# Kernel optimization log

Hardware: AMD Instinct MI355X
Metric: run time of the kernel (lower is better)

## Reference

```python
import math
import jax, jax.numpy as jnp
import numpy as np

B, NPC, K, D, T, L = 512, 32, 12, 64, 64, 4  # crystals, atoms/crystal, knn, node_dim, time_dim, layers
N = B * NPC
E_IN = 2 * D + 1 + T   # 193
N_IN = 2 * D + T       # 192


def setup_inputs() -> dict:
    key = jax.random.key(0)
    ks = jax.random.split(key, 32)
    rn = lambda k, shp, s=0.05: jax.random.normal(k, shp, jnp.float32) * s
    inp = {}
    inp["z_nodes"] = jax.random.normal(ks[0], (N, 128), jnp.float32)
    inp["t"] = jax.random.uniform(ks[1], (B,), jnp.float32) * 1000.0
    inp["frac_coords"] = jax.random.uniform(ks[2], (N, 3), jnp.float32)
    inp["lattice"] = jnp.eye(3, dtype=jnp.float32) * 5.0 + rn(ks[3], (B, 3, 3), 0.3)
    inp["batch_indices"] = jnp.repeat(jnp.arange(B, dtype=jnp.int32), NPC)
    inp["num_atoms"] = NPC
    # time_mlp: Linear(T, 2T) -> SiLU -> Linear(2T, T)
    inp["time_w1"] = rn(ks[4], (T, 2 * T)); inp["time_b1"] = rn(ks[5], (2 * T,))
    inp["time_w2"] = rn(ks[6], (2 * T, T)); inp["time_b2"] = rn(ks[7], (T,))
    # node_embedding: Linear(128, D)
    inp["emb_w"] = rn(ks[8], (128, D)); inp["emb_b"] = rn(ks[9], (D,))
    # per-layer EGNN params stacked on leading L axis
    inp["edge_w1"] = rn(ks[10], (L, E_IN, D)); inp["edge_b1"] = rn(ks[11], (L, D))
    inp["edge_w2"] = rn(ks[12], (L, D, D));    inp["edge_b2"] = rn(ks[13], (L, D))
    inp["coord_w1"] = rn(ks[14], (L, D, D));   inp["coord_b1"] = rn(ks[15], (L, D))
    inp["coord_w2"] = rn(ks[16], (L, D, 1))
    inp["node_w1"] = rn(ks[17], (L, N_IN, D)); inp["node_b1"] = rn(ks[18], (L, D))
    inp["node_w2"] = rn(ks[19], (L, D, D));    inp["node_b2"] = rn(ks[20], (L, D))
    return inp


def _forward(z_nodes, t, frac_coords, lattice, batch_indices, num_atoms,
             time_w1, time_b1, time_w2, time_b2, emb_w, emb_b,
             edge_w1, edge_b1, edge_w2, edge_b2, coord_w1, coord_b1, coord_w2,
             node_w1, node_b1, node_w2, node_b2):
    silu = jax.nn.silu
    n = num_atoms
    b = lattice.shape[0]
    n_nodes = z_nodes.shape[0]

    # ---- time embedding ----
    half = T // 2
    freqs = jnp.exp(jnp.arange(half, dtype=jnp.float32) * (-math.log(10000.0) / (half - 1)))
    ang = t[:, None] * freqs[None, :]
    sinu = jnp.concatenate([jnp.sin(ang), jnp.cos(ang)], axis=-1)  # [B, T]
    t_feat = silu(sinu @ time_w1 + time_b1) @ time_w2 + time_b2     # [B, T]
    t_nodes = t_feat[batch_indices]                                  # [N, T]

    h = z_nodes @ emb_w + emb_b                                      # [N, D]

    # ---- vectorized PBC KNN graph (all crystals have n atoms) ----
    f = frac_coords.reshape(b, n, 3)
    diff_f = f[:, :, None, :] - f[:, None, :, :]
    diff_f = diff_f - jnp.round(diff_f)
    diff_c = jnp.einsum('bijk,bkl->bijl', diff_f, lattice)           # [b,n,n,3]
    dist_sq = jnp.sum(diff_c * diff_c, axis=-1)                      # [b,n,n]
    dist_sq = jnp.where(jnp.eye(n, dtype=bool)[None], jnp.inf, dist_sq)
    k = min(K, n - 1)
    _, idx = jax.lax.top_k(-dist_sq, k)                              # [b,n,k] neighbor indices
    offs = (jnp.arange(b, dtype=jnp.int32) * n)[:, None, None]
    edge_src = (idx + offs).reshape(-1)                              # neighbors j
    edge_dst = (jnp.broadcast_to(jnp.arange(n, dtype=jnp.int32)[None, :, None], (b, n, k)) + offs).reshape(-1)
    diff_cart = jnp.take_along_axis(diff_c, jnp.broadcast_to(idx[..., None], (b, n, k, 3)), axis=2).reshape(-1, 3)
    dist_sq_e = jnp.take_along_axis(dist_sq, idx, axis=2).reshape(-1, 1)

    t_edges = t_nodes[edge_src]                                      # [E, T]

    total_shift = jnp.zeros((n_nodes, 3), dtype=h.dtype)
    for l in range(L):
        edge_in = jnp.concatenate([h[edge_src], h[edge_dst], dist_sq_e, t_edges], axis=-1)
        m = silu(edge_in @ edge_w1[l] + edge_b1[l])
        m = silu(m @ edge_w2[l] + edge_b2[l])                        # [E, D]
        cw = silu(m @ coord_w1[l] + coord_b1[l]) @ coord_w2[l]       # [E, 1]
        coord_update = jax.ops.segment_sum(diff_cart * cw, edge_src, num_segments=n_nodes)
        m_i = jax.ops.segment_sum(m, edge_dst, num_segments=n_nodes)
        node_in = jnp.concatenate([h, m_i, t_nodes], axis=-1)
        h = h + (silu(node_in @ node_w1[l] + node_b1[l]) @ node_w2[l] + node_b2[l])
        total_shift = total_shift + coord_update

    inv_lat = jnp.linalg.inv(lattice)[batch_indices]                 # [N,3,3]
    shift_frac = jnp.einsum('ni,nij->nj', total_shift, inv_lat)
    return shift_frac, h


def reference(z_nodes, t, frac_coords, lattice, batch_indices, num_atoms,
              time_w1, time_b1, time_w2, time_b2, emb_w, emb_b,
              edge_w1, edge_b1, edge_w2, edge_b2, coord_w1, coord_b1, coord_w2,
              node_w1, node_b1, node_w2, node_b2):
    return _forward(z_nodes, t, frac_coords, lattice, batch_indices, num_atoms,
                    time_w1, time_b1, time_w2, time_b2, emb_w, emb_b,
                    edge_w1, edge_b1, edge_w2, edge_b2, coord_w1, coord_b1, coord_w2,
                    node_w1, node_b1, node_w2, node_b2)
```

## Files before the change

### kernel.cpp

```cpp
#include <hip/hip_runtime.h>
#include <hip/hip_bf16.h>
#include <math.h>

#define NB 512
#define NPC 32
#define KNN 12
#define NL 4
#define NN (NB*NPC)
#define WPL 28672

typedef float v4f __attribute__((ext_vector_type(4)));
typedef short s8v __attribute__((ext_vector_type(8)));

__device__ __forceinline__ float silu_f(float x) {
    return x * __builtin_amdgcn_rcpf(1.0f + __builtin_amdgcn_exp2f(x * -1.44269504088896341f));
}

__device__ __forceinline__ unsigned short f2bf(float x) {
    unsigned u = __float_as_uint(x);
    u += 0x7fffu + ((u >> 16) & 1u);
    return (unsigned short)(u >> 16);
}

__device__ __forceinline__ unsigned pk2bf(float a, float b) {
    __hip_bfloat162 t = __float22bfloat162_rn(make_float2(a, b));
    union { __hip_bfloat162 h; unsigned u; } c; c.h = t;
    return c.u;
}

__device__ __forceinline__ int div12(int e) { return (e * 1366) >> 14; }

template<int R>
__device__ __forceinline__ void gemm_acc(const float* A, int astride,
                                         const float* __restrict__ Wg,
                                         int K, int lane, float* acc) {
#pragma unroll 2
    for (int kq = 0; kq < (K >> 2); ++kq) {
        float w0 = Wg[(4*kq+0)*64 + lane];
        float w1 = Wg[(4*kq+1)*64 + lane];
        float w2 = Wg[(4*kq+2)*64 + lane];
        float w3 = Wg[(4*kq+3)*64 + lane];
#pragma unroll
        for (int r = 0; r < R; ++r) {
            float4 a = *(const float4*)(A + r*astride + 4*kq);
            acc[r] = fmaf(a.x, w0, acc[r]);
            acc[r] = fmaf(a.y, w1, acc[r]);
            acc[r] = fmaf(a.z, w2, acc[r]);
            acc[r] = fmaf(a.w, w3, acc[r]);
        }
    }
}

extern "C" __global__ void prepack_w(const float* __restrict__ edge_w1, const float* __restrict__ edge_w2,
                                     const float* __restrict__ coord_w1, const float* __restrict__ node_w1,
                                     const float* __restrict__ node_w2, unsigned short* __restrict__ wout) {
    int g = blockIdx.x * 256 + threadIdx.x;
    if (g >= 4 * WPL / 8) return;
    int l = (g * 8) / WPL;
    int r = (g * 8) % WPL;
    int base, nKt, mat;
    if      (r < 8192)  { base = 0;     nKt = 2; mat = 0; }
    else if (r < 12288) { base = 8192;  nKt = 2; mat = 1; }
    else if (r < 16384) { base = 12288; nKt = 2; mat = 2; }
    else if (r < 24576) { base = 16384; nKt = 4; mat = 3; }
    else                { base = 24576; nKt = 2; mat = 4; }
    int idx = r - base;
    int lane = (idx >> 3) & 63, t = idx >> 9;
    int kt = t % nKt, nt = t / nKt;
    int k0 = kt*32 + ((lane >> 4) & 3)*8;
    int n  = nt*16 + (lane & 15);
    unsigned short o[8];
#pragma unroll
    for (int j = 0; j < 8; ++j) {
        int k = k0 + j;
        float v;
        if      (mat == 0) v = (n < 64) ? edge_w1[l*193*64 + k*64 + n] : edge_w1[l*193*64 + (64+k)*64 + (n-64)];
        else if (mat == 1) v = edge_w2 [l*4096 + k*64 + n];
        else if (mat == 2) v = coord_w1[l*4096 + k*64 + n];
        else if (mat == 3) v = node_w1 [l*192*64 + k*64 + n];
        else               v = node_w2 [l*4096 + k*64 + n];
        o[j] = f2bf(v);
    }
    *(s8v*)(wout + g*8) = *(s8v*)o;
}

extern "C" __global__ __launch_bounds__(512, 2)
void crystal_fused(const float* __restrict__ z_nodes, const float* __restrict__ t_in,
                   const float* __restrict__ frac,    const float* __restrict__ lattice,
                   const float* __restrict__ time_w1, const float* __restrict__ time_b1,
                   const float* __restrict__ time_w2, const float* __restrict__ time_b2,
                   const float* __restrict__ emb_w,   const float* __restrict__ emb_b,
                   const float* __restrict__ edge_w1, const float* __restrict__ edge_b1,
                   const float* __restrict__ edge_b2, const float* __restrict__ coord_b1,
                   const float* __restrict__ coord_w2,
                   const float* __restrict__ node_w1, const float* __restrict__ node_b1,
                   const float* __restrict__ node_b2,
                   const unsigned short* __restrict__ wbf,
                   float* __restrict__ out)
{
    __shared__ __align__(16) float s_h[32*65];
    __shared__ __align__(16) unsigned short s_habf[32*136];
    __shared__ __align__(16) unsigned short s_n1bf[32*72];
    __shared__ __align__(16) float s_hs[32*68];
    __shared__ __align__(16) float s_hd[32*68];
    __shared__ __align__(16) unsigned short s_tiles16[8*1152];
    __shared__ float s_dsq[32][33];
    __shared__ float2 s_emeta[384];
    __shared__ float s_endc[384*3];
    __shared__ float s_frac[32][3];
    __shared__ float s_lat[9], s_inv[9];
    __shared__ float s_sinu[64], s_t1[128], s_tf[64];
    __shared__ float s_tb4[NL*64], s_nb4[NL*64];
    __shared__ float s_shift[32*3];

    const int tid  = threadIdx.x;
    const int c    = blockIdx.x;
    const int lane = tid & 63;
    const int wave = tid >> 6;
    const int q4   = lane >> 4;
    const int c16  = lane & 15;
    const int base = c * NPC;

    if (tid < 96) {
        ((float*)s_frac)[tid] = frac[base*3 + tid];
    } else if (tid < 105) {
        s_lat[tid-96] = lattice[c*9 + (tid-96)];
    } else if (tid >= 128 && tid < 160) {
        int i = tid - 128;
        float freq = expf((float)i * (-9.210340371976184f / 31.0f));
        float ang  = t_in[c] * freq;
        s_sinu[i]    = sinf(ang);
        s_sinu[i+32] = cosf(ang);
    }
    __syncthreads();

    float* dcf = (float*)s_tiles16;
    {
        float l00=s_lat[0],l01=s_lat[1],l02=s_lat[2];
        float l10=s_lat[3],l11=s_lat[4],l12=s_lat[5];
        float l20=s_lat[6],l21=s_lat[7],l22=s_lat[8];
        for (int p = tid; p < 1024; p += 512) {
            int i = p >> 5, j = p & 31;
            float dx = s_frac[i][0]-s_frac[j][0];
            float dy = s_frac[i][1]-s_frac[j][1];
            float dz = s_frac[i][2]-s_frac[j][2];
            dx -= rintf(dx); dy -= rintf(dy); dz -= rintf(dz);
            float cx = dx*l00 + dy*l10 + dz*l20;
            float cy = dx*l01 + dy*l11 + dz*l21;
            float cz = dx*l02 + dy*l12 + dz*l22;
            float dd = cx*cx + cy*cy + cz*cz;
            s_dsq[i][j] = (i==j) ? 3.0e38f : dd;
            dcf[p*3+0]=cx; dcf[p*3+1]=cy; dcf[p*3+2]=cz;
        }
    }
    __syncthreads();

    if (tid < 32) {
        int i = tid;
        for (int k = 0; k < KNN; ++k) {
            float best = 3.9e38f; int bj = 0;
            for (int j = 0; j < 32; ++j) {
                float v = s_dsq[i][j];
                if (v < best) { best = v; bj = j; }
            }
            s_dsq[i][bj] = 3.9e38f;
            int e = i*KNN + k;
            s_emeta[e] = make_float2(best, __int_as_float(bj));
            int p = (i<<5) + bj;
            s_endc[e*3+0] = dcf[p*3+0];
            s_endc[e*3+1] = dcf[p*3+1];
            s_endc[e*3+2] = dcf[p*3+2];
        }
    } else if (tid >= 128 && tid < 256) {
        int jj = tid - 128;
        float p0 = time_b1[jj], p1=0.f, p2=0.f, p3=0.f;
        for (int k = 0; k < 64; k += 4) {
            p0 = fmaf(s_sinu[k+0], time_w1[(k+0)*128+jj], p0);
            p1 = fmaf(s_sinu[k+1], time_w1[(k+1)*128+jj], p1);
            p2 = fmaf(s_sinu[k+2], time_w1[(k+2)*128+jj], p2);
            p3 = fmaf(s_sinu[k+3], time_w1[(k+3)*128+jj], p3);
        }
        s_t1[jj] = silu_f((p0+p1) + (p2+p3));
    }
    __syncthreads();

    if (tid < 64) {
        float p0=time_b2[tid],p1=0.f,p2=0.f,p3=0.f;
        for (int k = 0; k < 128; k += 4) {
            p0 = fmaf(s_t1[k+0], time_w2[(k+0)*64+tid], p0);
            p1 = fmaf(s_t1[k+1], time_w2[(k+1)*64+tid], p1);
            p2 = fmaf(s_t1[k+2], time_w2[(k+2)*64+tid], p2);
            p3 = fmaf(s_t1[k+3], time_w2[(k+3)*64+tid], p3);
        }
        s_tf[tid] = (p0+p1) + (p2+p3);
    } else if (tid < 160) {
        s_shift[tid-64] = 0.0f;
    }
    __syncthreads();

    float* zbuf = (float*)s_tiles16;
    for (int q = tid; q < 4096; q += 512) zbuf[q] = z_nodes[base*128 + q];
    {
        int l = wave >> 1, kind = wave & 1;
        const float* Wt = kind ? (node_w1 + l*192*64 + 128*64) : (edge_w1 + l*193*64 + 129*64);
        const float* bb = kind ? (node_b1 + l*64) : (edge_b1 + l*64);
        float p0 = bb[lane], p1=0.f, p2=0.f, p3=0.f;
        for (int k = 0; k < 64; k += 4) {
            p0 = fmaf(s_tf[k+0], Wt[(k+0)*64 + lane], p0);
            p1 = fmaf(s_tf[k+1], Wt[(k+1)*64 + lane], p1);
            p2 = fmaf(s_tf[k+2], Wt[(k+2)*64 + lane], p2);
            p3 = fmaf(s_tf[k+3], Wt[(k+3)*64 + lane], p3);
        }
        float v = (p0+p1) + (p2+p3);
        if (kind) s_nb4[l*64 + lane] = v;
        else      s_tb4[l*64 + lane] = v;
    }
    __syncthreads();

    {
        float acc[4];
#pragma unroll
        for (int r = 0; r < 4; ++r) acc[r] = emb_b[lane];
        gemm_acc<4>(zbuf + (wave*4)*128, 128, emb_w, 128, lane, acc);
#pragma unroll
        for (int r = 0; r < 4; ++r) {
            int row = wave*4 + r;
            s_h[row*65 + lane] = acc[r];
            s_habf[row*136 + lane] = f2bf(acc[r]);
        }
    }
    __syncthreads();

    for (int l = 0; l < NL; ++l) {
        const unsigned short* wl = wbf + l*WPL;
        const float* w1row = edge_w1 + l*193*64 + 128*64;
        float b2e_v[4], cb1_v[4], w2c_v[4];
#pragma unroll
        for (int nt = 0; nt < 4; ++nt) {
            b2e_v[nt] = edge_b2 [l*64 + nt*16 + c16];
            cb1_v[nt] = coord_b1[l*64 + nt*16 + c16];
            w2c_v[nt] = coord_w2[l*64 + nt*16 + c16];
        }

        {
            s8v a[2][2];
#pragma unroll
            for (int mt = 0; mt < 2; ++mt)
#pragma unroll
                for (int kt = 0; kt < 2; ++kt)
                    a[mt][kt] = *(const s8v*)(s_habf + (mt*16 + c16)*136 + kt*32 + q4*8);
            v4f acc[2] = {{0.f,0.f,0.f,0.f},{0.f,0.f,0.f,0.f}};
#pragma unroll
            for (int kt = 0; kt < 2; ++kt) {
                s8v b = *(const s8v*)(wl + ((wave*2+kt)*64 + lane)*8);
#pragma unroll
                for (int mt = 0; mt < 2; ++mt)
                    acc[mt] = __builtin_amdgcn_mfma_f32_16x16x32_bf16(a[mt][kt], b, acc[mt], 0, 0, 0);
            }
            int col = wave*16 + c16;
            if (wave < 4) {
#pragma unroll
                for (int mt = 0; mt < 2; ++mt)
#pragma unroll
                    for (int reg = 0; reg < 4; ++reg)
                        s_hs[(mt*16 + q4*4 + reg)*68 + col] = acc[mt][reg];
            } else {
                int colb = col - 64;
                float tbv = s_tb4[l*64 + colb];
#pragma unroll
                for (int mt = 0; mt < 2; ++mt)
#pragma unroll
                    for (int reg = 0; reg < 4; ++reg)
                        s_hd[(mt*16 + q4*4 + reg)*68 + colb] = acc[mt][reg] + tbv;
            }
        }
        __syncthreads();

        {
            s8v w2f[8], wc1f[8];
#pragma unroll
            for (int nt = 0; nt < 4; ++nt)
#pragma unroll
                for (int kt = 0; kt < 2; ++kt) {
                    w2f [nt*2+kt] = *(const s8v*)(wl +  8192 + ((nt*2+kt)*64 + lane)*8);
                    wc1f[nt*2+kt] = *(const s8v*)(wl + 12288 + ((nt*2+kt)*64 + lane)*8);
                }
            union F4 { float4 v; float f[4]; };
            F4 W4[4];
            W4[0].v = *(const float4*)(w1row + q4*8);
            W4[1].v = *(const float4*)(w1row + q4*8 + 4);
            W4[2].v = *(const float4*)(w1row + 32 + q4*8);
            W4[3].v = *(const float4*)(w1row + 32 + q4*8 + 4);

            unsigned short* tile = s_tiles16 + wave*1152;
            float miacc[4][4];
#pragma unroll
            for (int a2 = 0; a2 < 4; ++a2)
#pragma unroll
                for (int b2 = 0; b2 < 4; ++b2) miacc[a2][b2] = 0.f;

#pragma unroll
            for (int m = 0; m < 3; ++m) {
                const int e0g = wave*48 + m*16;
                const int eL  = e0g + c16;
                float2 me = s_emeta[eL];
                int srcn = __float_as_int(me.y);
                int dstn = div12(eL);
                float dq = me.x;
                const float* hsr = s_hs + srcn*68 + q4*8;
                const float* hdr = s_hd + dstn*68 + q4*8;
                F4 H[4], G[4];
                H[0].v = *(const float4*)(hsr);      H[1].v = *(const float4*)(hsr+4);
                H[2].v = *(const float4*)(hsr+32);   H[3].v = *(const float4*)(hsr+36);
                G[0].v = *(const float4*)(hdr);      G[1].v = *(const float4*)(hdr+4);
                G[2].v = *(const float4*)(hdr+32);   G[3].v = *(const float4*)(hdr+36);
                union S8 { s8v v; unsigned u[4]; } A0, A1;
#pragma unroll
                for (int g2 = 0; g2 < 4; ++g2) {
                    float s0 = silu_f(fmaf(dq, W4[g2].f[0], H[g2].f[0] + G[g2].f[0]));
                    float s1 = silu_f(fmaf(dq, W4[g2].f[1], H[g2].f[1] + G[g2].f[1]));
                    float s2 = silu_f(fmaf(dq, W4[g2].f[2], H[g2].f[2] + G[g2].f[2]));
                    float s3 = silu_f(fmaf(dq, W4[g2].f[3], H[g2].f[3] + G[g2].f[3]));
                    unsigned lo = pk2bf(s0, s1), hi2 = pk2bf(s2, s3);
                    if (g2 < 2) { A0.u[g2*2] = lo; A0.u[g2*2+1] = hi2; }
                    else        { A1.u[(g2-2)*2] = lo; A1.u[(g2-2)*2+1] = hi2; }
                }

                const int thr = (m==0) ? 3 : (m==1) ? 2 : 1;
                const int dlo = m;
#pragma unroll
                for (int nt = 0; nt < 4; ++nt) {
                    v4f acc = {0.f,0.f,0.f,0.f};
                    acc = __builtin_amdgcn_mfma_f32_16x16x32_bf16(A0.v, w2f[nt*2+0], acc, 0,0,0);
                    acc = __builtin_amdgcn_mfma_f32_16x16x32_bf16(A1.v, w2f[nt*2+1], acc, 0,0,0);
                    int col = nt*16 + c16;
                    float msum = 0.f;
#pragma unroll
                    for (int reg = 0; reg < 4; ++reg) {
                        float v = silu_f(acc[reg] + b2e_v[nt]);
                        tile[(q4*4 + reg)*72 + col] = f2bf(v);
                        msum += v;
                    }
                    bool hi = (q4 >= thr);
                    miacc[nt][dlo]   += hi ? 0.f : msum;
                    miacc[nt][dlo+1] += hi ? msum : 0.f;
                }
                asm volatile("s_waitcnt lgkmcnt(0)" ::: "memory");
                s8v c0 = *(const s8v*)(tile + c16*72 +      q4*8);
                s8v c1 = *(const s8v*)(tile + c16*72 + 32 + q4*8);
                float cwp[4] = {0.f,0.f,0.f,0.f};
#pragma unroll
                for (int nt = 0; nt < 4; ++nt) {
                    v4f acc = {0.f,0.f,0.f,0.f};
                    acc = __builtin_amdgcn_mfma_f32_16x16x32_bf16(c0, wc1f[nt*2+0], acc, 0,0,0);
                    acc = __builtin_amdgcn_mfma_f32_16x16x32_bf16(c1, wc1f[nt*2+1], acc, 0,0,0);
#pragma unroll
                    for (int reg = 0; reg < 4; ++reg)
                        cwp[reg] += silu_f(acc[reg] + cb1_v[nt]) * w2c_v[nt];
                }
#pragma unroll
                for (int reg = 0; reg < 4; ++reg) {
                    float v = cwp[reg];
                    v += __shfl_xor(v, 1); v += __shfl_xor(v, 2);
                    v += __shfl_xor(v, 4); v += __shfl_xor(v, 8);
                    int e = e0g + q4*4 + reg;
                    if (c16 < 3) {
                        int src = __float_as_int(s_emeta[e].y);
                        atomicAdd(&s_shift[src*3 + c16], s_endc[e*3 + c16] * v);
                    }
                }
            }
#pragma unroll
            for (int nt = 0; nt < 4; ++nt)
#pragma unroll
                for (int d = 0; d < 4; ++d) {
                    float v = miacc[nt][d];
                    v += __shfl_xor(v, 16);
                    v += __shfl_xor(v, 32);
                    s_habf[(wave*4 + d)*136 + 64 + nt*16 + c16] = f2bf(v);
                }
        }
        __syncthreads();

        {
            int mt = wave & 1, nt = wave >> 1;
            int col = nt*16 + c16;
            float nbc = s_nb4[l*64 + col];
            v4f acc = {0.f,0.f,0.f,0.f};
#pragma unroll
            for (int kt = 0; kt < 4; ++kt) {
                s8v b = *(const s8v*)(wl + 16384 + ((nt*4+kt)*64 + lane)*8);
                s8v a = *(const s8v*)(s_habf + (mt*16 + c16)*136 + kt*32 + q4*8);
                acc = __builtin_amdgcn_mfma_f32_16x16x32_bf16(a, b, acc, 0,0,0);
            }
#pragma unroll
            for (int reg = 0; reg < 4; ++reg) {
                int row = mt*16 + q4*4 + reg;
                s_n1bf[row*72 + col] = f2bf(silu_f(acc[reg] + nbc));
            }
        }
        __syncthreads();

        {
            int mt = wave & 1, nt = wave >> 1;
            s8v b0 = *(const s8v*)(wl + 24576 + ((nt*2+0)*64 + lane)*8);
            s8v b1 = *(const s8v*)(wl + 24576 + ((nt*2+1)*64 + lane)*8);
            int col = nt*16 + c16;
            float nb2_v = node_b2[l*64 + col];
            s8v a0 = *(const s8v*)(s_n1bf + (mt*16 + c16)*72 +      q4*8);
            s8v a1 = *(const s8v*)(s_n1bf + (mt*16 + c16)*72 + 32 + q4*8);
            v4f acc = {0.f,0.f,0.f,0.f};
            acc = __builtin_amdgcn_mfma_f32_16x16x32_bf16(a0, b0, acc, 0,0,0);
            acc = __builtin_amdgcn_mfma_f32_16x16x32_bf16(a1, b1, acc, 0,0,0);
#pragma unroll
            for (int reg = 0; reg < 4; ++reg) {
                int row = mt*16 + q4*4 + reg;
                float hn = s_h[row*65 + col] + acc[reg] + nb2_v;
                s_h[row*65 + col] = hn;
                s_habf[row*136 + col] = f2bf(hn);
            }
        }
        __syncthreads();
    }

    if (tid == 0) {
        float a=s_lat[0],b=s_lat[1],cc=s_lat[2];
        float d=s_lat[3],e=s_lat[4],f =s_lat[5];
        float g=s_lat[6],h2=s_lat[7],i2=s_lat[8];
        float A  =  (e*i2 - f*h2);
        float Bm = -(d*i2 - f*g);
        float C  =  (d*h2 - e*g);
        float det = a*A + b*Bm + cc*C;
        float rd = 1.0f/det;
        s_inv[0] = A*rd;
        s_inv[1] = -(b*i2 - cc*h2)*rd;
        s_inv[2] =  (b*f  - cc*e )*rd;
        s_inv[3] = Bm*rd;
        s_inv[4] =  (a*i2 - cc*g )*rd;
        s_inv[5] = -(a*f  - cc*d )*rd;
        s_inv[6] = C*rd;
        s_inv[7] = -(a*h2 - b*g  )*rd;
        s_inv[8] =  (a*e  - b*d  )*rd;
    }
    __syncthreads();
    if (tid < 96) {
        int r = tid/3, j = tid%3;
        float v = s_shift[r*3+0]*s_inv[0*3+j]
                + s_shift[r*3+1]*s_inv[1*3+j]
                + s_shift[r*3+2]*s_inv[2*3+j];
        out[(base + r)*3 + j] = v;
    }
    for (int q = tid; q < 2048; q += 512) {
        int row = q >> 6, colq = q & 63;
        out[NN*3 + base*64 + q] = s_h[row*65 + colq];
    }
}

extern "C" void kernel_launch(void* const* d_in, const int* in_sizes, int n_in,
                              void* d_out, int out_size, void* d_ws, size_t ws_size,
                              hipStream_t stream) {
    unsigned short* wbf = (unsigned short*)d_ws;
    prepack_w<<<(4*WPL/8 + 255)/256, 256, 0, stream>>>(
        (const float*)d_in[12], (const float*)d_in[14], (const float*)d_in[16],
        (const float*)d_in[19], (const float*)d_in[21], wbf);
    crystal_fused<<<NB, 512, 0, stream>>>(
        (const float*)d_in[0],  (const float*)d_in[1],  (const float*)d_in[2],  (const float*)d_in[3],
        (const float*)d_in[6],  (const float*)d_in[7],  (const float*)d_in[8],  (const float*)d_in[9],
        (const float*)d_in[10], (const float*)d_in[11],
        (const float*)d_in[12], (const float*)d_in[13], (const float*)d_in[15],
        (const float*)d_in[17], (const float*)d_in[18],
        (const float*)d_in[19], (const float*)d_in[20], (const float*)d_in[22],
        wbf, (float*)d_out);
}
```

Baseline: 219.8 us.

## Raise occupancy bound and cut register pressure in edge loop

Changes launch bounds from 2 to 4 blocks per SM-equivalent, forcing the compiler to fit in about half the VGPRs. To make that fit, the coord_w1 weight fragments are no longer held in registers across the edge loop but reloaded from global memory each iteration inside a non-unrolled loop. The w1 row and h loads are split into two scoped halves to shorten live ranges. This trades more global/L2 loads and less unrolling, plus possible spills, for higher occupancy to hide latency.

```diff
diff --git a/kernel.cpp b/kernel.cpp
--- a/kernel.cpp
+++ b/kernel.cpp
@@ -84,7 +84,7 @@
     *(s8v*)(wout + g*8) = *(s8v*)o;
 }
 
-extern "C" __global__ __launch_bounds__(512, 2)
+extern "C" __global__ __launch_bounds__(512, 4)
 void crystal_fused(const float* __restrict__ z_nodes, const float* __restrict__ t_in,
                    const float* __restrict__ frac,    const float* __restrict__ lattice,
                    const float* __restrict__ time_w1, const float* __restrict__ time_b1,
@@ -234,13 +234,13 @@
     for (int l = 0; l < NL; ++l) {
         const unsigned short* wl = wbf + l*WPL;
         const float* w1row = edge_w1 + l*193*64 + 128*64;
-        float b2e_v[4], cb1_v[4], w2c_v[4];
-#pragma unroll
-        for (int nt = 0; nt < 4; ++nt) {
-            b2e_v[nt] = edge_b2 [l*64 + nt*16 + c16];
-            cb1_v[nt] = coord_b1[l*64 + nt*16 + c16];
-            w2c_v[nt] = coord_w2[l*64 + nt*16 + c16];
-        }
+        float b2e_v[4];
+#pragma unroll
+        for (int nt = 0; nt < 4; ++nt) b2e_v[nt] = edge_b2[l*64 + nt*16 + c16];
+        const float cb10 = coord_b1[l*64 +  0 + c16], cb11 = coord_b1[l*64 + 16 + c16];
+        const float cb12 = coord_b1[l*64 + 32 + c16], cb13 = coord_b1[l*64 + 48 + c16];
+        const float w2c0 = coord_w2[l*64 +  0 + c16], w2c1 = coord_w2[l*64 + 16 + c16];
+        const float w2c2 = coord_w2[l*64 + 32 + c16], w2c3 = coord_w2[l*64 + 48 + c16];
 
         {
             s8v a[2][2];
@@ -277,20 +277,12 @@
         __syncthreads();
 
         {
-            s8v w2f[8], wc1f[8];
+            s8v w2f[8];
 #pragma unroll
             for (int nt = 0; nt < 4; ++nt)
 #pragma unroll
-                for (int kt = 0; kt < 2; ++kt) {
-                    w2f [nt*2+kt] = *(const s8v*)(wl +  8192 + ((nt*2+kt)*64 + lane)*8);
-                    wc1f[nt*2+kt] = *(const s8v*)(wl + 12288 + ((nt*2+kt)*64 + lane)*8);
-                }
-            union F4 { float4 v; float f[4]; };
-            F4 W4[4];
-            W4[0].v = *(const float4*)(w1row + q4*8);
-            W4[1].v = *(const float4*)(w1row + q4*8 + 4);
-            W4[2].v = *(const float4*)(w1row + 32 + q4*8);
-            W4[3].v = *(const float4*)(w1row + 32 + q4*8 + 4);
+                for (int kt = 0; kt < 2; ++kt)
+                    w2f[nt*2+kt] = *(const s8v*)(wl + 8192 + ((nt*2+kt)*64 + lane)*8);
 
             unsigned short* tile = s_tiles16 + wave*1152;
             float miacc[4][4];
@@ -309,21 +301,38 @@
                 float dq = me.x;
                 const float* hsr = s_hs + srcn*68 + q4*8;
                 const float* hdr = s_hd + dstn*68 + q4*8;
-                F4 H[4], G[4];
-                H[0].v = *(const float4*)(hsr);      H[1].v = *(const float4*)(hsr+4);
-                H[2].v = *(const float4*)(hsr+32);   H[3].v = *(const float4*)(hsr+36);
-                G[0].v = *(const float4*)(hdr);      G[1].v = *(const float4*)(hdr+4);
-                G[2].v = *(const float4*)(hdr+32);   G[3].v = *(const float4*)(hdr+36);
                 union S8 { s8v v; unsigned u[4]; } A0, A1;
-#pragma unroll
-                for (int g2 = 0; g2 < 4; ++g2) {
-                    float s0 = silu_f(fmaf(dq, W4[g2].f[0], H[g2].f[0] + G[g2].f[0]));
-                    float s1 = silu_f(fmaf(dq, W4[g2].f[1], H[g2].f[1] + G[g2].f[1]));
-                    float s2 = silu_f(fmaf(dq, W4[g2].f[2], H[g2].f[2] + G[g2].f[2]));
-                    float s3 = silu_f(fmaf(dq, W4[g2].f[3], H[g2].f[3] + G[g2].f[3]));
-                    unsigned lo = pk2bf(s0, s1), hi2 = pk2bf(s2, s3);
-                    if (g2 < 2) { A0.u[g2*2] = lo; A0.u[g2*2+1] = hi2; }
-                    else        { A1.u[(g2-2)*2] = lo; A1.u[(g2-2)*2+1] = hi2; }
+                {
+                    float4 w0 = *(const float4*)(w1row + q4*8);
+                    float4 w1 = *(const float4*)(w1row + q4*8 + 4);
+                    float4 h0 = *(const float4*)(hsr);
+                    float4 h1 = *(const float4*)(hsr + 4);
+                    float4 g0 = *(const float4*)(hdr);
+                    float4 g1 = *(const float4*)(hdr + 4);
+                    A0.u[0] = pk2bf(silu_f(fmaf(dq, w0.x, h0.x + g0.x)),
+                                    silu_f(fmaf(dq, w0.y, h0.y + g0.y)));
+                    A0.u[1] = pk2bf(silu_f(fmaf(dq, w0.z, h0.z + g0.z)),
+                                    silu_f(fmaf(dq, w0.w, h0.w + g0.w)));
+                    A0.u[2] = pk2bf(silu_f(fmaf(dq, w1.x, h1.x + g1.x)),
+                                    silu_f(fmaf(dq, w1.y, h1.y + g1.y)));
+                    A0.u[3] = pk2bf(silu_f(fmaf(dq, w1.z, h1.z + g1.z)),
+                                    silu_f(fmaf(dq, w1.w, h1.w + g1.w)));
+                }
+                {
+                    float4 w2 = *(const float4*)(w1row + 32 + q4*8);
+                    float4 w3 = *(const float4*)(w1row + 32 + q4*8 + 4);
+                    float4 h2 = *(const float4*)(hsr + 32);
+                    float4 h3 = *(const float4*)(hsr + 36);
+                    float4 g2 = *(const float4*)(hdr + 32);
+                    float4 g3 = *(const float4*)(hdr + 36);
+                    A1.u[0] = pk2bf(silu_f(fmaf(dq, w2.x, h2.x + g2.x)),
+                                    silu_f(fmaf(dq, w2.y, h2.y + g2.y)));
+                    A1.u[1] = pk2bf(silu_f(fmaf(dq, w2.z, h2.z + g2.z)),
+                                    silu_f(fmaf(dq, w2.w, h2.w + g2.w)));
+                    A1.u[2] = pk2bf(silu_f(fmaf(dq, w3.x, h3.x + g3.x)),
+                                    silu_f(fmaf(dq, w3.y, h3.y + g3.y)));
+                    A1.u[3] = pk2bf(silu_f(fmaf(dq, w3.z, h3.z + g3.z)),
+                                    silu_f(fmaf(dq, w3.w, h3.w + g3.w)));
                 }
 
                 const int thr = (m==0) ? 3 : (m==1) ? 2 : 1;
@@ -349,14 +358,18 @@
                 s8v c0 = *(const s8v*)(tile + c16*72 +      q4*8);
                 s8v c1 = *(const s8v*)(tile + c16*72 + 32 + q4*8);
                 float cwp[4] = {0.f,0.f,0.f,0.f};
-#pragma unroll
+#pragma unroll 1
                 for (int nt = 0; nt < 4; ++nt) {
+                    s8v b0 = *(const s8v*)(wl + 12288 + ((nt*2+0)*64 + lane)*8);
+                    s8v b1 = *(const s8v*)(wl + 12288 + ((nt*2+1)*64 + lane)*8);
                     v4f acc = {0.f,0.f,0.f,0.f};
-                    acc = __builtin_amdgcn_mfma_f32_16x16x32_bf16(c0, wc1f[nt*2+0], acc, 0,0,0);
-                    acc = __builtin_amdgcn_mfma_f32_16x16x32_bf16(c1, wc1f[nt*2+1], acc, 0,0,0);
+                    acc = __builtin_amdgcn_mfma_f32_16x16x32_bf16(c0, b0, acc, 0,0,0);
+                    acc = __builtin_amdgcn_mfma_f32_16x16x32_bf16(c1, b1, acc, 0,0,0);
+                    float cb1 = (nt==0) ? cb10 : (nt==1) ? cb11 : (nt==2) ? cb12 : cb13;
+                    float w2c = (nt==0) ? w2c0 : (nt==1) ? w2c1 : (nt==2) ? w2c2 : w2c3;
 #pragma unroll
                     for (int reg = 0; reg < 4; ++reg)
-                        cwp[reg] += silu_f(acc[reg] + cb1_v[nt]) * w2c_v[nt];
+                        cwp[reg] += silu_f(acc[reg] + cb1) * w2c;
                 }
 #pragma unroll
                 for (int reg = 0; reg < 4; ++reg) {
```

New measurement: 228.2 us. 1.04x slower.
